# Performance work log

Measured on AMD Instinct MI355X. Metric: run time of the kernel, lower is better.

Reference implementation:

```python
import jax, jax.numpy as jnp
import numpy as np
import math

R1 = 1.0
R2 = 4.0
NBINS_XY = 4
NBINS_ZY = 4
PARTITIONS = NBINS_XY * NBINS_ZY * 2  # 32
TOPK = 200
TWO_PI = 2.0 * math.pi
PI = math.pi


def setup_inputs() -> dict:
    key = jax.random.key(0)
    k1, k2 = jax.random.split(key)
    # LiDAR-like coordinates, ~[-30, 30] meters
    sampled_vehicle_points = jax.random.normal(k1, (1024, 3), dtype=jnp.float32) * 20.0
    fusion_point = jax.random.normal(k2, (20000, 3), dtype=jnp.float32) * 20.0
    return {"sampled_vehicle_points": sampled_vehicle_points, "fusion_point": fusion_point}


def _compute_partitions_batch(q):
    # q: [S, K, 3]. rel[b, i, j] = q[b, j] - q[b, i]  (A.unsqueeze(1) - B.unsqueeze(2))
    rel = q[:, None, :, :] - q[:, :, None, :]  # [S, K, K, 3]
    angles_xy = jnp.fmod(jnp.arctan2(rel[..., 1], rel[..., 0]) + TWO_PI, TWO_PI)
    angles_zy = jnp.fmod(jnp.arctan2(rel[..., 1], rel[..., 2]) + TWO_PI, PI)
    xy_bins = jnp.floor(angles_xy / (TWO_PI / NBINS_XY))
    zy_bins = jnp.floor(angles_zy / (PI / NBINS_ZY))
    # hash(A, B, seed=NBINS_ZY): -1 where either < 0
    angle_ok = (xy_bins >= 0) & (zy_bins >= 0)
    angles_bins = jnp.where(angle_ok, xy_bins * NBINS_ZY + zy_bins, -1.0)
    D = jnp.sqrt(jnp.sum(rel * rel, axis=-1) + 1e-7)  # [S, K, K]
    dist_bins = jnp.where(D >= R2, 1.0, jnp.where(D >= R1, 0.0, -1.0))
    bin_ok = (dist_bins >= 0) & (angles_bins >= 0)
    bins = jnp.where(bin_ok, dist_bins * (NBINS_XY * NBINS_ZY) + angles_bins, -1.0)
    return bins  # [S, K, K] float, -1 for ignored


def reference(sampled_vehicle_points, fusion_point):
    # kNN query: K nearest fusion points for each sampled vehicle point
    d2 = jnp.sum(
        (sampled_vehicle_points[:, None, :] - fusion_point[None, :, :]) ** 2, axis=-1
    )  # [S, Nf]
    _, idx = jax.lax.top_k(-d2, TOPK)  # indices of TOPK smallest distances
    queried = fusion_point[idx]  # [S, K, 3]

    bins = _compute_partitions_batch(queried)  # [S, K, K]
    row0 = bins[:, 0, :]  # [S, K] — only row 0 is used by the loss
    # points_in_partition[s, p] = sum_j (row0[s, j] == p) + 1
    counts = jnp.sum(
        row0[:, :, None] == jnp.arange(PARTITIONS, dtype=bins.dtype)[None, None, :],
        axis=1,
    ).astype(jnp.float32) + 1.0  # [S, P]
    pip = counts / jnp.linalg.norm(counts, axis=-1, keepdims=True) * 4.0
    gt_dist = jax.nn.softmax(pip, axis=-1)
    return gt_dist
```

## Files before the change

### kernel.cpp

```cpp
#include <hip/hip_runtime.h>
#include <math.h>

#define KTOP 200
#define NPART 32
#define BLOCK 512
#define NHIST 2048
#define CAND_CAP 512
#define WCAP 512
#define CLIST_CAP 1536
#define SRANK_MIN 64u

__device__ __forceinline__ float d2_ref(float ax, float ay, float az,
                                        float bx, float by, float bz) {
    float dx = __fsub_rn(ax, bx), dy = __fsub_rn(ay, by), dz = __fsub_rn(az, bz);
    return __fadd_rn(__fadd_rn(__fmul_rn(dx, dx), __fmul_rn(dy, dy)), __fmul_rn(dz, dz));
}

__device__ __forceinline__ unsigned key_of(const float* __restrict__ fus, int j,
                                           float vx, float vy, float vz) {
    return __float_as_uint(d2_ref(vx, vy, vz, fus[3*j], fus[3*j+1], fus[3*j+2]));
}

__device__ __forceinline__ int compute_bin(float rx, float ry, float rz) {
    const float TWO_PI_F = (float)6.283185307179586;
    const float PI_F     = (float)3.141592653589793;
    const float XY_W     = (float)(6.283185307179586 / 4.0);
    const float ZY_W     = (float)(3.141592653589793 / 4.0);

    float d2 = __fadd_rn(__fadd_rn(__fmul_rn(rx, rx), __fmul_rn(ry, ry)), __fmul_rn(rz, rz));
    float D  = sqrtf(__fadd_rn(d2, 1e-7f));
    float dist_bin;
    if (D >= 4.0f)      dist_bin = 1.0f;
    else if (D >= 1.0f) dist_bin = 0.0f;
    else                return -1;

    float axy = fmodf(atan2f(ry, rx) + TWO_PI_F, TWO_PI_F);
    float azy = fmodf(atan2f(ry, rz) + TWO_PI_F, PI_F);
    float xyb = floorf(__fdiv_rn(axy, XY_W));
    float zyb = floorf(__fdiv_rn(azy, ZY_W));
    if (!(xyb >= 0.0f && zyb >= 0.0f)) return -1;
    float ab  = xyb * 4.0f + zyb;
    int bin = (int)(dist_bin * 16.0f + ab);
    return bin;
}

__global__ __launch_bounds__(BLOCK, 8)
void shape_context_kernel(const float* __restrict__ veh,
                          const float* __restrict__ fus,
                          float* __restrict__ out,
                          int nfus) {
    const int b   = blockIdx.x;
    const int tid = threadIdx.x;
    const int lane = tid & 63;
    const int wid  = tid >> 6;

    __shared__ unsigned int hist[NHIST];
    __shared__ unsigned long long clist[CLIST_CAP];
    __shared__ unsigned long long cand[CAND_CAP];
    __shared__ int wlist[WCAP];
    __shared__ unsigned int hist32[NPART];
    __shared__ unsigned int waveTot[BLOCK / 64];
    __shared__ unsigned int waveBase[BLOCK / 64];
    __shared__ unsigned int s_bucket, s_rem, s_bcount;
    __shared__ int s_candCount, s_wcount, s_clistCount;
    __shared__ float s_q0[3];
    __shared__ unsigned long long s_minPacked, s_lowBound;

    const float vx = veh[b * 3 + 0], vy = veh[b * 3 + 1], vz = veh[b * 3 + 2];
    const float4* fus4 = (const float4*)fus;
    const int ntrip = nfus >> 2;

    if (tid == 0) { s_minPacked = ~0ull; s_candCount = 0; s_wcount = 0; s_clistCount = 0; }
    for (int i = tid; i < NHIST; i += BLOCK) hist[i] = 0;
    if (tid < NPART) hist32[tid] = 0;
    __syncthreads();

    auto find_bucket = [&](unsigned remq) {
        if (tid == 0) s_bucket = 0xFFFFFFFFu;
        const int PER = NHIST / BLOCK;
        int base = tid * PER;
        unsigned p = 0;
        #pragma unroll
        for (int i = 0; i < PER; i++) p += hist[base + i];
        unsigned incl = p;
        #pragma unroll
        for (int d = 1; d < 64; d <<= 1) {
            unsigned n = __shfl_up(incl, d, 64);
            if (lane >= d) incl += n;
        }
        if (lane == 63) waveTot[wid] = incl;
        __syncthreads();
        if (tid == 0) {
            unsigned acc = 0;
            for (int w = 0; w < BLOCK / 64; w++) { waveBase[w] = acc; acc += waveTot[w]; }
        }
        __syncthreads();
        unsigned excl = waveBase[wid] + incl - p;
        if (excl < remq && remq <= excl + p) {
            unsigned cum = excl;
            #pragma unroll
            for (int i = 0; i < PER; i++) {
                unsigned c = hist[base + i];
                if (cum + c >= remq) { s_bucket = base + i; s_rem = remq - cum; s_bcount = c; break; }
                cum += c;
            }
        }
        __syncthreads();
    };

    auto push_l = [&](unsigned k, unsigned j) {
        int pos = atomicAdd(&s_clistCount, 1);
        if (pos < CLIST_CAP) clist[pos] = ((unsigned long long)k << 32) | j;
    };
    auto push_c = [&](unsigned k, unsigned j) {
        atomicAdd(&hist[k >> 21], 1u);
        int pos = atomicAdd(&s_clistCount, 1);
        if (pos < CLIST_CAP) clist[pos] = ((unsigned long long)k << 32) | j;
    };

    unsigned k0 = 0, k1 = 0, k2 = 0, k3 = 0;
    const bool t0v = (tid < ntrip);
    if (t0v) {
        float4 A = fus4[3 * tid], Bq = fus4[3 * tid + 1], Cq = fus4[3 * tid + 2];
        k0 = __float_as_uint(d2_ref(vx, vy, vz, A.x,  A.y,  A.z));
        k1 = __float_as_uint(d2_ref(vx, vy, vz, A.w,  Bq.x, Bq.y));
        k2 = __float_as_uint(d2_ref(vx, vy, vz, Bq.z, Bq.w, Cq.x));
        k3 = __float_as_uint(d2_ref(vx, vy, vz, Cq.y, Cq.z, Cq.w));
        atomicAdd(&hist[k0 >> 21], 1u);
        atomicAdd(&hist[k1 >> 21], 1u);
        atomicAdd(&hist[k2 >> 21], 1u);
        atomicAdd(&hist[k3 >> 21], 1u);
    }
    __syncthreads();

    unsigned srank;
    {
        long long sample = (long long)((ntrip < BLOCK) ? ntrip : BLOCK) * 4;
        if (sample >= (long long)nfus) {
            srank = KTOP;
        } else {
            unsigned s2 = (unsigned)(((long long)3 * KTOP * sample + nfus - 1) / nfus);
            srank = (s2 < SRANK_MIN) ? SRANK_MIN : s2;
        }
    }
    find_bucket(srank);
    const unsigned E = (s_bucket < NHIST) ? s_bucket : (NHIST - 1);
    const unsigned maxKey = ((E + 1u) << 21) - 1u;

    if (t0v) {
        unsigned jb = 4u * (unsigned)tid;
        int qm = (k0 <= maxKey ? 1 : 0) | (k1 <= maxKey ? 2 : 0)
               | (k2 <= maxKey ? 4 : 0) | (k3 <= maxKey ? 8 : 0);
        if (qm) {
            if (qm & 1) push_l(k0, jb + 0);
            if (qm & 2) push_l(k1, jb + 1);
            if (qm & 4) push_l(k2, jb + 2);
            if (qm & 8) push_l(k3, jb + 3);
        }
    }

    {
        int m = BLOCK + tid;
        bool valid = (m < ntrip);
        float4 A, Bq, Cq;
        if (valid) { A = fus4[3 * m]; Bq = fus4[3 * m + 1]; Cq = fus4[3 * m + 2]; }
        while (valid) {
            const int mn = m + BLOCK;
            const bool vnext = (mn < ntrip);
            float4 An, Bn, Cn;
            if (vnext) { An = fus4[3 * mn]; Bn = fus4[3 * mn + 1]; Cn = fus4[3 * mn + 2]; }

            unsigned q0k = __float_as_uint(d2_ref(vx, vy, vz, A.x,  A.y,  A.z));
            unsigned q1k = __float_as_uint(d2_ref(vx, vy, vz, A.w,  Bq.x, Bq.y));
            unsigned q2k = __float_as_uint(d2_ref(vx, vy, vz, Bq.z, Bq.w, Cq.x));
            unsigned q3k = __float_as_uint(d2_ref(vx, vy, vz, Cq.y, Cq.z, Cq.w));
            int qm = (q0k <= maxKey ? 1 : 0) | (q1k <= maxKey ? 2 : 0)
                   | (q2k <= maxKey ? 4 : 0) | (q3k <= maxKey ? 8 : 0);
            if (qm) {
                unsigned jb = 4u * (unsigned)m;
                if (qm & 1) push_c(q0k, jb + 0);
                if (qm & 2) push_c(q1k, jb + 1);
                if (qm & 4) push_c(q2k, jb + 2);
                if (qm & 8) push_c(q3k, jb + 3);
            }
            A = An; Bq = Bn; Cq = Cn; m = mn; valid = vnext;
        }
    }
    for (int j = (nfus & ~3) + tid; j < nfus; j += BLOCK) {
        unsigned k = key_of(fus, j, vx, vy, vz);
        if (k <= maxKey) push_c(k, (unsigned)j);
    }
    __syncthreads();

    find_bucket(KTOP);
    unsigned T = s_bucket;
    unsigned rem = s_rem;
    unsigned bcount = s_bcount;
    int shift = 21;
    const bool fastOK = (s_clistCount <= CLIST_CAP) && (T <= E);

    if (fastOK) {
        const int cn = s_clistCount;
        unsigned long long lm = ~0ull;
        for (int i = tid; i < cn; i += BLOCK) { unsigned long long p = clist[i]; lm = (p < lm) ? p : lm; }
        #pragma unroll
        for (int d = 32; d > 0; d >>= 1) {
            unsigned long long o = __shfl_xor(lm, d, 64);
            lm = (o < lm) ? o : lm;
        }
        if (lane == 0) atomicMin(&s_minPacked, lm);
        __syncthreads();
    } else {
        for (int i = tid; i < NHIST; i += BLOCK) hist[i] = 0;
        __syncthreads();
        unsigned long long lm = ~0ull;
        for (int j = tid; j < nfus; j += BLOCK) {
            unsigned k = key_of(fus, j, vx, vy, vz);
            atomicAdd(&hist[k >> 21], 1u);
            unsigned long long p = ((unsigned long long)k << 32) | (unsigned)j;
            lm = (p < lm) ? p : lm;
        }
        #pragma unroll
        for (int d = 32; d > 0; d >>= 1) {
            unsigned long long o = __shfl_xor(lm, d, 64);
            lm = (o < lm) ? o : lm;
        }
        if (lane == 0) atomicMin(&s_minPacked, lm);
        __syncthreads();
        find_bucket(KTOP);
        T = s_bucket; rem = s_rem; bcount = s_bcount;
    }

    if (tid == 0) {
        int idx0 = (int)(s_minPacked & 0xFFFFFFFFull);
        s_q0[0] = fus[idx0 * 3]; s_q0[1] = fus[idx0 * 3 + 1]; s_q0[2] = fus[idx0 * 3 + 2];
    }
    __syncthreads();
    const float q0x = s_q0[0], q0y = s_q0[1], q0z = s_q0[2];

    while (bcount > CAND_CAP && shift > 0) {
        int newshift = (shift > 11) ? (shift - 11) : 0;
        unsigned digmask = (1u << (shift - newshift)) - 1;
        for (int i = tid; i < NHIST; i += BLOCK) hist[i] = 0;
        __syncthreads();
        for (int j = tid; j < nfus; j += BLOCK) {
            unsigned k = key_of(fus, j, vx, vy, vz);
            if ((k >> shift) == T) atomicAdd(&hist[(k >> newshift) & digmask], 1u);
        }
        __syncthreads();
        find_bucket(rem);
        T = (T << (shift - newshift)) | s_bucket;
        rem = s_rem;
        bcount = s_bcount;
        shift = newshift;
    }

    if (fastOK && shift == 21) {
        const int cn = s_clistCount;
        for (int i = tid; i < cn; i += BLOCK) {
            unsigned long long p = clist[i];
            unsigned hi = (unsigned)(p >> 53);
            if (hi < T) {
                int pos = atomicAdd(&s_wcount, 1);
                if (pos < WCAP) wlist[pos] = (int)(p & 0xFFFFFFFFull);
            } else if (hi == T) {
                int pos = atomicAdd(&s_candCount, 1);
                if (pos < CAND_CAP) cand[pos] = p;
            }
        }
    } else {
        for (int j = tid; j < nfus; j += BLOCK) {
            unsigned k = key_of(fus, j, vx, vy, vz);
            unsigned hi = k >> shift;
            if (hi < T) { int pos = atomicAdd(&s_wcount, 1); if (pos < WCAP) wlist[pos] = j; }
            else if (hi == T) { int pos = atomicAdd(&s_candCount, 1); if (pos < CAND_CAP) cand[pos] = ((unsigned long long)k << 32) | (unsigned)j; }
        }
    }
    __syncthreads();

    const int cnt = s_candCount;
    if (cnt <= CAND_CAP) {
        for (int i = tid; i < cnt; i += BLOCK) {
            unsigned long long me = cand[i];
            int rank = 0;
            for (int k2 = 0; k2 < cnt; k2++) rank += (cand[k2] < me) ? 1 : 0;
            if (rank < (int)rem) {
                int pos = atomicAdd(&s_wcount, 1);
                if (pos < WCAP) wlist[pos] = (int)(me & 0xFFFFFFFFull);
            }
        }
    }
    __syncthreads();

    {
        int wc = s_wcount; if (wc > WCAP) wc = WCAP;
        for (int i = tid; i < wc; i += BLOCK) {
            int j = wlist[i];
            float fx = fus[3 * j], fy = fus[3 * j + 1], fz = fus[3 * j + 2];
            int bin = compute_bin(__fsub_rn(fx, q0x), __fsub_rn(fy, q0y), __fsub_rn(fz, q0z));
            if (bin >= 0 && bin < NPART) atomicAdd(&hist32[bin], 1u);
        }
    }
    __syncthreads();

    if (cnt > CAND_CAP) {
        if (tid == 0) s_lowBound = 0;
        __syncthreads();
        for (unsigned itx = 0; itx < rem; ++itx) {
            if (tid == 0) s_minPacked = ~0ull;
            __syncthreads();
            unsigned long long lowB = s_lowBound;
            unsigned long long lm = ~0ull;
            for (int j = tid; j < nfus; j += BLOCK) {
                unsigned k = key_of(fus, j, vx, vy, vz);
                if ((k >> shift) == T) {
                    unsigned long long p = ((unsigned long long)k << 32) | (unsigned)j;
                    if (p >= lowB && p < lm) lm = p;
                }
            }
            #pragma unroll
            for (int d = 32; d > 0; d >>= 1) {
                unsigned long long o = __shfl_xor(lm, d, 64);
                lm = (o < lm) ? o : lm;
            }
            if (lane == 0) atomicMin(&s_minPacked, lm);
            __syncthreads();
            if (tid == 0) {
                int jm = (int)(s_minPacked & 0xFFFFFFFFull);
                float fx = fus[jm * 3], fy = fus[jm * 3 + 1], fz = fus[jm * 3 + 2];
                int bin = compute_bin(__fsub_rn(fx, q0x), __fsub_rn(fy, q0y), __fsub_rn(fz, q0z));
                if (bin >= 0 && bin < NPART) hist32[bin] += 1u;
                s_lowBound = s_minPacked + 1;
            }
            __syncthreads();
        }
    }

    if (tid < NPART) {
        float c = (float)hist32[tid] + 1.0f;
        float ss = __fmul_rn(c, c);
        #pragma unroll
        for (int d = 16; d > 0; d >>= 1) ss += __shfl_xor(ss, d, 64);
        float v = __fmul_rn(__fdiv_rn(c, sqrtf(ss)), 4.0f);
        float mx = v;
        #pragma unroll
        for (int d = 16; d > 0; d >>= 1) mx = fmaxf(mx, __shfl_xor(mx, d, 64));
        float e = expf(v - mx);
        float sum = e;
        #pragma unroll
        for (int d = 16; d > 0; d >>= 1) sum += __shfl_xor(sum, d, 64);
        out[b * NPART + tid] = __fdiv_rn(e, sum);
    }
}

extern "C" void kernel_launch(void* const* d_in, const int* in_sizes, int n_in,
                              void* d_out, int out_size, void* d_ws, size_t ws_size,
                              hipStream_t stream) {
    const float* veh = (const float*)d_in[0];
    const float* fus = (const float*)d_in[1];
    float* out = (float*)d_out;
    int nveh = in_sizes[0] / 3;
    int nfus = in_sizes[1] / 3;
    shape_context_kernel<<<nveh, BLOCK, 0, stream>>>(veh, fus, out, nfus);
}
```

Baseline: 77.05 us.

## Stage fusion point chunks through LDS for coalesced loads in kNN scan

Replaces per-thread strided float4 triplet loads with fully coalesced chunk loads of 3*BLOCK float4s that are staged into a shared-memory pool, then each thread computes distances from LDS. The cand/wlist arrays are aliased onto that pool to keep LDS usage bounded. Launch bounds occupancy hint is lowered from 8 to 6. This adds two block barriers per chunk and removes the register-level prefetch of the next chunk, so latency hiding now depends on occupancy; the aliasing assumes cand/wlist are only used after the scan.

```diff
diff --git a/kernel.cpp b/kernel.cpp
--- a/kernel.cpp
+++ b/kernel.cpp
@@ -9,6 +9,8 @@
 #define WCAP 512
 #define CLIST_CAP 1536
 #define SRANK_MIN 64u
+#define CHUNK_PTS (4 * BLOCK)
+#define CHUNK_F4  (3 * BLOCK)
 
 __device__ __forceinline__ float d2_ref(float ax, float ay, float az,
                                         float bx, float by, float bz) {
@@ -44,7 +46,7 @@
     return bin;
 }
 
-__global__ __launch_bounds__(BLOCK, 8)
+__global__ __launch_bounds__(BLOCK, 6)
 void shape_context_kernel(const float* __restrict__ veh,
                           const float* __restrict__ fus,
                           float* __restrict__ out,
@@ -56,8 +58,7 @@
 
     __shared__ unsigned int hist[NHIST];
     __shared__ unsigned long long clist[CLIST_CAP];
-    __shared__ unsigned long long cand[CAND_CAP];
-    __shared__ int wlist[WCAP];
+    __shared__ __align__(16) char s_pool[CHUNK_F4 * 16];
     __shared__ unsigned int hist32[NPART];
     __shared__ unsigned int waveTot[BLOCK / 64];
     __shared__ unsigned int waveBase[BLOCK / 64];
@@ -66,9 +67,14 @@
     __shared__ float s_q0[3];
     __shared__ unsigned long long s_minPacked, s_lowBound;
 
+    float4* stage4 = (float4*)s_pool;
+    const float* stagef = (const float*)s_pool;
+    unsigned long long* cand = (unsigned long long*)s_pool;
+    int* wlist = (int*)(s_pool + CAND_CAP * 8);
+
     const float vx = veh[b * 3 + 0], vy = veh[b * 3 + 1], vz = veh[b * 3 + 2];
     const float4* fus4 = (const float4*)fus;
-    const int ntrip = nfus >> 2;
+    const int nfull = nfus / CHUNK_PTS;
 
     if (tid == 0) { s_minPacked = ~0ull; s_candCount = 0; s_wcount = 0; s_clistCount = 0; }
     for (int i = tid; i < NHIST; i += BLOCK) hist[i] = 0;
@@ -118,14 +124,21 @@
         if (pos < CLIST_CAP) clist[pos] = ((unsigned long long)k << 32) | j;
     };
 
+    auto key_at = [&](int p) {
+        float x = stagef[3 * p], y = stagef[3 * p + 1], z = stagef[3 * p + 2];
+        return __float_as_uint(d2_ref(vx, vy, vz, x, y, z));
+    };
+
+    const bool have0 = (nfull > 0);
     unsigned k0 = 0, k1 = 0, k2 = 0, k3 = 0;
-    const bool t0v = (tid < ntrip);
-    if (t0v) {
-        float4 A = fus4[3 * tid], Bq = fus4[3 * tid + 1], Cq = fus4[3 * tid + 2];
-        k0 = __float_as_uint(d2_ref(vx, vy, vz, A.x,  A.y,  A.z));
-        k1 = __float_as_uint(d2_ref(vx, vy, vz, A.w,  Bq.x, Bq.y));
-        k2 = __float_as_uint(d2_ref(vx, vy, vz, Bq.z, Bq.w, Cq.x));
-        k3 = __float_as_uint(d2_ref(vx, vy, vz, Cq.y, Cq.z, Cq.w));
+    if (have0) {
+        float4 r0 = fus4[tid], r1 = fus4[BLOCK + tid], r2 = fus4[2 * BLOCK + tid];
+        stage4[tid] = r0; stage4[BLOCK + tid] = r1; stage4[2 * BLOCK + tid] = r2;
+        __syncthreads();
+        k0 = key_at(tid);
+        k1 = key_at(tid + BLOCK);
+        k2 = key_at(tid + 2 * BLOCK);
+        k3 = key_at(tid + 3 * BLOCK);
         atomicAdd(&hist[k0 >> 21], 1u);
         atomicAdd(&hist[k1 >> 21], 1u);
         atomicAdd(&hist[k2 >> 21], 1u);
@@ -135,7 +148,7 @@
 
     unsigned srank;
     {
-        long long sample = (long long)((ntrip < BLOCK) ? ntrip : BLOCK) * 4;
+        long long sample = have0 ? (long long)CHUNK_PTS : 0;
         if (sample >= (long long)nfus) {
             srank = KTOP;
         } else {
@@ -147,46 +160,34 @@
     const unsigned E = (s_bucket < NHIST) ? s_bucket : (NHIST - 1);
     const unsigned maxKey = ((E + 1u) << 21) - 1u;
 
-    if (t0v) {
-        unsigned jb = 4u * (unsigned)tid;
-        int qm = (k0 <= maxKey ? 1 : 0) | (k1 <= maxKey ? 2 : 0)
-               | (k2 <= maxKey ? 4 : 0) | (k3 <= maxKey ? 8 : 0);
-        if (qm) {
-            if (qm & 1) push_l(k0, jb + 0);
-            if (qm & 2) push_l(k1, jb + 1);
-            if (qm & 4) push_l(k2, jb + 2);
-            if (qm & 8) push_l(k3, jb + 3);
-        }
-    }
-
-    {
-        int m = BLOCK + tid;
-        bool valid = (m < ntrip);
-        float4 A, Bq, Cq;
-        if (valid) { A = fus4[3 * m]; Bq = fus4[3 * m + 1]; Cq = fus4[3 * m + 2]; }
-        while (valid) {
-            const int mn = m + BLOCK;
-            const bool vnext = (mn < ntrip);
-            float4 An, Bn, Cn;
-            if (vnext) { An = fus4[3 * mn]; Bn = fus4[3 * mn + 1]; Cn = fus4[3 * mn + 2]; }
-
-            unsigned q0k = __float_as_uint(d2_ref(vx, vy, vz, A.x,  A.y,  A.z));
-            unsigned q1k = __float_as_uint(d2_ref(vx, vy, vz, A.w,  Bq.x, Bq.y));
-            unsigned q2k = __float_as_uint(d2_ref(vx, vy, vz, Bq.z, Bq.w, Cq.x));
-            unsigned q3k = __float_as_uint(d2_ref(vx, vy, vz, Cq.y, Cq.z, Cq.w));
-            int qm = (q0k <= maxKey ? 1 : 0) | (q1k <= maxKey ? 2 : 0)
-                   | (q2k <= maxKey ? 4 : 0) | (q3k <= maxKey ? 8 : 0);
-            if (qm) {
-                unsigned jb = 4u * (unsigned)m;
-                if (qm & 1) push_c(q0k, jb + 0);
-                if (qm & 2) push_c(q1k, jb + 1);
-                if (qm & 4) push_c(q2k, jb + 2);
-                if (qm & 8) push_c(q3k, jb + 3);
-            }
-            A = An; Bq = Bn; Cq = Cn; m = mn; valid = vnext;
-        }
-    }
-    for (int j = (nfus & ~3) + tid; j < nfus; j += BLOCK) {
+    if (have0) {
+        if (k0 <= maxKey) push_l(k0, (unsigned)tid);
+        if (k1 <= maxKey) push_l(k1, (unsigned)(tid + BLOCK));
+        if (k2 <= maxKey) push_l(k2, (unsigned)(tid + 2 * BLOCK));
+        if (k3 <= maxKey) push_l(k3, (unsigned)(tid + 3 * BLOCK));
+    }
+
+    for (int c = 1; c < nfull; ++c) {
+        const int f4b = c * CHUNK_F4;
+        float4 r0 = fus4[f4b + tid];
+        float4 r1 = fus4[f4b + BLOCK + tid];
+        float4 r2 = fus4[f4b + 2 * BLOCK + tid];
+        __syncthreads();
+        stage4[tid] = r0; stage4[BLOCK + tid] = r1; stage4[2 * BLOCK + tid] = r2;
+        __syncthreads();
+        const int jb = c * CHUNK_PTS;
+        unsigned q0 = key_at(tid);
+        unsigned q1 = key_at(tid + BLOCK);
+        unsigned q2 = key_at(tid + 2 * BLOCK);
+        unsigned q3 = key_at(tid + 3 * BLOCK);
+        if ((q0 <= maxKey) | (q1 <= maxKey) | (q2 <= maxKey) | (q3 <= maxKey)) {
+            if (q0 <= maxKey) push_c(q0, (unsigned)(jb + tid));
+            if (q1 <= maxKey) push_c(q1, (unsigned)(jb + tid + BLOCK));
+            if (q2 <= maxKey) push_c(q2, (unsigned)(jb + tid + 2 * BLOCK));
+            if (q3 <= maxKey) push_c(q3, (unsigned)(jb + tid + 3 * BLOCK));
+        }
+    }
+    for (int j = nfull * CHUNK_PTS + tid; j < nfus; j += BLOCK) {
         unsigned k = key_of(fus, j, vx, vy, vz);
         if (k <= maxKey) push_c(k, (unsigned)j);
     }
```

New measurement: 89.23 us. 15.8% more time.

## Process four query points per block to reuse fusion-point loads

Applied to the files above, without the earlier changes.

Each block now handles four vehicle points instead of one. Every loaded fusion-point triple is scored against all four queries, with a separate histogram and candidate list kept per query. The block size rises from 512 to 1024 threads and the grid shrinks to a quarter. This cuts global load traffic and per-block setup, at the cost of more shared memory, more registers, only 256 blocks for the GPU, and the per-query selection tails running one after another.

```diff
diff --git a/kernel.cpp b/kernel.cpp
--- a/kernel.cpp
+++ b/kernel.cpp
@@ -3,7 +3,8 @@
 
 #define KTOP 200
 #define NPART 32
-#define BLOCK 512
+#define BLOCK 1024
+#define NV 4
 #define NHIST 2048
 #define CAND_CAP 512
 #define WCAP 512
@@ -14,6 +15,11 @@
                                         float bx, float by, float bz) {
     float dx = __fsub_rn(ax, bx), dy = __fsub_rn(ay, by), dz = __fsub_rn(az, bz);
     return __fadd_rn(__fadd_rn(__fmul_rn(dx, dx), __fmul_rn(dy, dy)), __fmul_rn(dz, dz));
+}
+
+__device__ __forceinline__ unsigned key2(float cx, float cy, float cz,
+                                         float px, float py, float pz) {
+    return __float_as_uint(d2_ref(cx, cy, cz, px, py, pz));
 }
 
 __device__ __forceinline__ unsigned key_of(const float* __restrict__ fus, int j,
@@ -44,44 +50,51 @@
     return bin;
 }
 
-__global__ __launch_bounds__(BLOCK, 8)
+__global__ __launch_bounds__(BLOCK, 4)
 void shape_context_kernel(const float* __restrict__ veh,
                           const float* __restrict__ fus,
                           float* __restrict__ out,
-                          int nfus) {
-    const int b   = blockIdx.x;
-    const int tid = threadIdx.x;
+                          int nfus, int nveh) {
+    const int b    = blockIdx.x;
+    const int tid  = threadIdx.x;
     const int lane = tid & 63;
     const int wid  = tid >> 6;
-
-    __shared__ unsigned int hist[NHIST];
-    __shared__ unsigned long long clist[CLIST_CAP];
+    const int vbase = b * NV;
+
+    __shared__ unsigned int hist[NV][NHIST];
+    __shared__ unsigned long long clist[NV][CLIST_CAP];
     __shared__ unsigned long long cand[CAND_CAP];
     __shared__ int wlist[WCAP];
     __shared__ unsigned int hist32[NPART];
     __shared__ unsigned int waveTot[BLOCK / 64];
     __shared__ unsigned int waveBase[BLOCK / 64];
     __shared__ unsigned int s_bucket, s_rem, s_bcount;
-    __shared__ int s_candCount, s_wcount, s_clistCount;
+    __shared__ int s_candCount, s_wcount, s_clistCount[NV];
+    __shared__ unsigned int s_E[NV];
     __shared__ float s_q0[3];
     __shared__ unsigned long long s_minPacked, s_lowBound;
 
-    const float vx = veh[b * 3 + 0], vy = veh[b * 3 + 1], vz = veh[b * 3 + 2];
+    const int vi0 = min(vbase + 0, nveh - 1), vi1 = min(vbase + 1, nveh - 1),
+              vi2 = min(vbase + 2, nveh - 1), vi3 = min(vbase + 3, nveh - 1);
+    const float cAx = veh[vi0*3], cAy = veh[vi0*3+1], cAz = veh[vi0*3+2];
+    const float cBx = veh[vi1*3], cBy = veh[vi1*3+1], cBz = veh[vi1*3+2];
+    const float cCx = veh[vi2*3], cCy = veh[vi2*3+1], cCz = veh[vi2*3+2];
+    const float cDx = veh[vi3*3], cDy = veh[vi3*3+1], cDz = veh[vi3*3+2];
+
     const float4* fus4 = (const float4*)fus;
     const int ntrip = nfus >> 2;
 
-    if (tid == 0) { s_minPacked = ~0ull; s_candCount = 0; s_wcount = 0; s_clistCount = 0; }
-    for (int i = tid; i < NHIST; i += BLOCK) hist[i] = 0;
-    if (tid < NPART) hist32[tid] = 0;
-    __syncthreads();
-
-    auto find_bucket = [&](unsigned remq) {
+    for (int i = tid; i < NV * NHIST; i += BLOCK) ((unsigned*)hist)[i] = 0;
+    if (tid < NV) s_clistCount[tid] = 0;
+    __syncthreads();
+
+    auto find_bucket = [&](const unsigned* h, unsigned remq) {
         if (tid == 0) s_bucket = 0xFFFFFFFFu;
         const int PER = NHIST / BLOCK;
         int base = tid * PER;
         unsigned p = 0;
         #pragma unroll
-        for (int i = 0; i < PER; i++) p += hist[base + i];
+        for (int i = 0; i < PER; i++) p += h[base + i];
         unsigned incl = p;
         #pragma unroll
         for (int d = 1; d < 64; d <<= 1) {
@@ -100,7 +113,7 @@
             unsigned cum = excl;
             #pragma unroll
             for (int i = 0; i < PER; i++) {
-                unsigned c = hist[base + i];
+                unsigned c = h[base + i];
                 if (cum + c >= remq) { s_bucket = base + i; s_rem = remq - cum; s_bcount = c; break; }
                 cum += c;
             }
@@ -108,216 +121,156 @@
         __syncthreads();
     };
 
-    auto push_l = [&](unsigned k, unsigned j) {
-        int pos = atomicAdd(&s_clistCount, 1);
-        if (pos < CLIST_CAP) clist[pos] = ((unsigned long long)k << 32) | j;
+    auto push_l = [&](int v, unsigned k, unsigned j) {
+        int pos = atomicAdd(&s_clistCount[v], 1);
+        if (pos < CLIST_CAP) clist[v][pos] = ((unsigned long long)k << 32) | j;
     };
-    auto push_c = [&](unsigned k, unsigned j) {
-        atomicAdd(&hist[k >> 21], 1u);
-        int pos = atomicAdd(&s_clistCount, 1);
-        if (pos < CLIST_CAP) clist[pos] = ((unsigned long long)k << 32) | j;
+    auto push_c = [&](int v, unsigned k, unsigned j) {
+        atomicAdd(&hist[v][k >> 21], 1u);
+        int pos = atomicAdd(&s_clistCount[v], 1);
+        if (pos < CLIST_CAP) clist[v][pos] = ((unsigned long long)k << 32) | j;
     };
 
-    unsigned k0 = 0, k1 = 0, k2 = 0, k3 = 0;
-    const bool t0v = (tid < ntrip);
+    const int t0n = (ntrip < BLOCK) ? ntrip : BLOCK;
+    const bool t0v = (tid < t0n);
+    float p0x=0,p0y=0,p0z=0, p1x=0,p1y=0,p1z=0, p2x=0,p2y=0,p2z=0, p3x=0,p3y=0,p3z=0;
+    unsigned sA0=0,sA1=0,sA2=0,sA3=0, sB0=0,sB1=0,sB2=0,sB3=0;
+    unsigned sC0=0,sC1=0,sC2=0,sC3=0, sD0=0,sD1=0,sD2=0,sD3=0;
     if (t0v) {
-        float4 A = fus4[3 * tid], Bq = fus4[3 * tid + 1], Cq = fus4[3 * tid + 2];
-        k0 = __float_as_uint(d2_ref(vx, vy, vz, A.x,  A.y,  A.z));
-        k1 = __float_as_uint(d2_ref(vx, vy, vz, A.w,  Bq.x, Bq.y));
-        k2 = __float_as_uint(d2_ref(vx, vy, vz, Bq.z, Bq.w, Cq.x));
-        k3 = __float_as_uint(d2_ref(vx, vy, vz, Cq.y, Cq.z, Cq.w));
-        atomicAdd(&hist[k0 >> 21], 1u);
-        atomicAdd(&hist[k1 >> 21], 1u);
-        atomicAdd(&hist[k2 >> 21], 1u);
-        atomicAdd(&hist[k3 >> 21], 1u);
+        float4 A = fus4[3*tid], Bq = fus4[3*tid+1], Cq = fus4[3*tid+2];
+        p0x=A.x;  p0y=A.y;  p0z=A.z;
+        p1x=A.w;  p1y=Bq.x; p1z=Bq.y;
+        p2x=Bq.z; p2y=Bq.w; p2z=Cq.x;
+        p3x=Cq.y; p3y=Cq.z; p3z=Cq.w;
+        sA0=key2(cAx,cAy,cAz,p0x,p0y,p0z); sA1=key2(cAx,cAy,cAz,p1x,p1y,p1z);
+        sA2=key2(cAx,cAy,cAz,p2x,p2y,p2z); sA3=key2(cAx,cAy,cAz,p3x,p3y,p3z);
+        sB0=key2(cBx,cBy,cBz,p0x,p0y,p0z); sB1=key2(cBx,cBy,cBz,p1x,p1y,p1z);
+        sB2=key2(cBx,cBy,cBz,p2x,p2y,p2z); sB3=key2(cBx,cBy,cBz,p3x,p3y,p3z);
+        sC0=key2(cCx,cCy,cCz,p0x,p0y,p0z); sC1=key2(cCx,cCy,cCz,p1x,p1y,p1z);
+        sC2=key2(cCx,cCy,cCz,p2x,p2y,p2z); sC3=key2(cCx,cCy,cCz,p3x,p3y,p3z);
+        sD0=key2(cDx,cDy,cDz,p0x,p0y,p0z); sD1=key2(cDx,cDy,cDz,p1x,p1y,p1z);
+        sD2=key2(cDx,cDy,cDz,p2x,p2y,p2z); sD3=key2(cDx,cDy,cDz,p3x,p3y,p3z);
+        atomicAdd(&hist[0][sA0>>21],1u); atomicAdd(&hist[0][sA1>>21],1u);
+        atomicAdd(&hist[0][sA2>>21],1u); atomicAdd(&hist[0][sA3>>21],1u);
+        atomicAdd(&hist[1][sB0>>21],1u); atomicAdd(&hist[1][sB1>>21],1u);
+        atomicAdd(&hist[1][sB2>>21],1u); atomicAdd(&hist[1][sB3>>21],1u);
+        atomicAdd(&hist[2][sC0>>21],1u); atomicAdd(&hist[2][sC1>>21],1u);
+        atomicAdd(&hist[2][sC2>>21],1u); atomicAdd(&hist[2][sC3>>21],1u);
+        atomicAdd(&hist[3][sD0>>21],1u); atomicAdd(&hist[3][sD1>>21],1u);
+        atomicAdd(&hist[3][sD2>>21],1u); atomicAdd(&hist[3][sD3>>21],1u);
     }
     __syncthreads();
 
     unsigned srank;
     {
-        long long sample = (long long)((ntrip < BLOCK) ? ntrip : BLOCK) * 4;
+        long long sample = 4LL * t0n;
         if (sample >= (long long)nfus) {
             srank = KTOP;
         } else {
-            unsigned s2 = (unsigned)(((long long)3 * KTOP * sample + nfus - 1) / nfus);
+            unsigned s2 = (unsigned)((3LL * KTOP * sample + nfus - 1) / nfus);
             srank = (s2 < SRANK_MIN) ? SRANK_MIN : s2;
         }
     }
-    find_bucket(srank);
-    const unsigned E = (s_bucket < NHIST) ? s_bucket : (NHIST - 1);
-    const unsigned maxKey = ((E + 1u) << 21) - 1u;
+    find_bucket(hist[0], srank);
+    const unsigned E0 = (s_bucket < NHIST) ? s_bucket : (NHIST-1);
+    if (tid == 0) s_E[0] = E0;
+    __syncthreads();
+    find_bucket(hist[1], srank);
+    const unsigned E1 = (s_bucket < NHIST) ? s_bucket : (NHIST-1);
+    if (tid == 0) s_E[1] = E1;
+    __syncthreads();
+    find_bucket(hist[2], srank);
+    const unsigned E2 = (s_bucket < NHIST) ? s_bucket : (NHIST-1);
+    if (tid == 0) s_E[2] = E2;
+    __syncthreads();
+    find_bucket(hist[3], srank);
+    const unsigned E3 = (s_bucket < NHIST) ? s_bucket : (NHIST-1);
+    if (tid == 0) s_E[3] = E3;
+    __syncthreads();
+    const unsigned mk0 = ((E0+1u)<<21)-1u, mk1 = ((E1+1u)<<21)-1u;
+    const unsigned mk2 = ((E2+1u)<<21)-1u, mk3 = ((E3+1u)<<21)-1u;
 
     if (t0v) {
         unsigned jb = 4u * (unsigned)tid;
-        int qm = (k0 <= maxKey ? 1 : 0) | (k1 <= maxKey ? 2 : 0)
-               | (k2 <= maxKey ? 4 : 0) | (k3 <= maxKey ? 8 : 0);
-        if (qm) {
-            if (qm & 1) push_l(k0, jb + 0);
-            if (qm & 2) push_l(k1, jb + 1);
-            if (qm & 4) push_l(k2, jb + 2);
-            if (qm & 8) push_l(k3, jb + 3);
-        }
-    }
-
-    {
-        int m = BLOCK + tid;
-        bool valid = (m < ntrip);
-        float4 A, Bq, Cq;
-        if (valid) { A = fus4[3 * m]; Bq = fus4[3 * m + 1]; Cq = fus4[3 * m + 2]; }
-        while (valid) {
-            const int mn = m + BLOCK;
-            const bool vnext = (mn < ntrip);
-            float4 An, Bn, Cn;
-            if (vnext) { An = fus4[3 * mn]; Bn = fus4[3 * mn + 1]; Cn = fus4[3 * mn + 2]; }
-
-            unsigned q0k = __float_as_uint(d2_ref(vx, vy, vz, A.x,  A.y,  A.z));
-            unsigned q1k = __float_as_uint(d2_ref(vx, vy, vz, A.w,  Bq.x, Bq.y));
-            unsigned q2k = __float_as_uint(d2_ref(vx, vy, vz, Bq.z, Bq.w, Cq.x));
-            unsigned q3k = __float_as_uint(d2_ref(vx, vy, vz, Cq.y, Cq.z, Cq.w));
-            int qm = (q0k <= maxKey ? 1 : 0) | (q1k <= maxKey ? 2 : 0)
-                   | (q2k <= maxKey ? 4 : 0) | (q3k <= maxKey ? 8 : 0);
-            if (qm) {
-                unsigned jb = 4u * (unsigned)m;
-                if (qm & 1) push_c(q0k, jb + 0);
-                if (qm & 2) push_c(q1k, jb + 1);
-                if (qm & 4) push_c(q2k, jb + 2);
-                if (qm & 8) push_c(q3k, jb + 3);
-            }
-            A = An; Bq = Bn; Cq = Cn; m = mn; valid = vnext;
+        if (sA0<=mk0) push_l(0,sA0,jb+0); if (sA1<=mk0) push_l(0,sA1,jb+1);
+        if (sA2<=mk0) push_l(0,sA2,jb+2); if (sA3<=mk0) push_l(0,sA3,jb+3);
+        if (sB0<=mk1) push_l(1,sB0,jb+0); if (sB1<=mk1) push_l(1,sB1,jb+1);
+        if (sB2<=mk1) push_l(1,sB2,jb+2); if (sB3<=mk1) push_l(1,sB3,jb+3);
+        if (sC0<=mk2) push_l(2,sC0,jb+0); if (sC1<=mk2) push_l(2,sC1,jb+1);
+        if (sC2<=mk2) push_l(2,sC2,jb+2); if (sC3<=mk2) push_l(2,sC3,jb+3);
+        if (sD0<=mk3) push_l(3,sD0,jb+0); if (sD1<=mk3) push_l(3,sD1,jb+1);
+        if (sD2<=mk3) push_l(3,sD2,jb+2); if (sD3<=mk3) push_l(3,sD3,jb+3);
+    }
+
+    for (int m = BLOCK + tid; m < ntrip; m += BLOCK) {
+        float4 A = fus4[3*m], Bq = fus4[3*m+1], Cq = fus4[3*m+2];
+        float x0=A.x,  y0=A.y,  z0=A.z;
+        float x1=A.w,  y1=Bq.x, z1=Bq.y;
+        float x2=Bq.z, y2=Bq.w, z2=Cq.x;
+        float x3=Cq.y, y3=Cq.z, z3=Cq.w;
+        unsigned jb = 4u * (unsigned)m;
+        {
+            unsigned k0=key2(cAx,cAy,cAz,x0,y0,z0), k1=key2(cAx,cAy,cAz,x1,y1,z1);
+            unsigned k2=key2(cAx,cAy,cAz,x2,y2,z2), k3=key2(cAx,cAy,cAz,x3,y3,z3);
+            if ((k0<=mk0)|(k1<=mk0)|(k2<=mk0)|(k3<=mk0)) {
+                if (k0<=mk0) push_c(0,k0,jb+0); if (k1<=mk0) push_c(0,k1,jb+1);
+                if (k2<=mk0) push_c(0,k2,jb+2); if (k3<=mk0) push_c(0,k3,jb+3);
+            }
+        }
+        {
+            unsigned k0=key2(cBx,cBy,cBz,x0,y0,z0), k1=key2(cBx,cBy,cBz,x1,y1,z1);
+            unsigned k2=key2(cBx,cBy,cBz,x2,y2,z2), k3=key2(cBx,cBy,cBz,x3,y3,z3);
+            if ((k0<=mk1)|(k1<=mk1)|(k2<=mk1)|(k3<=mk1)) {
+                if (k0<=mk1) push_c(1,k0,jb+0); if (k1<=mk1) push_c(1,k1,jb+1);
+                if (k2<=mk1) push_c(1,k2,jb+2); if (k3<=mk1) push_c(1,k3,jb+3);
+            }
+        }
+        {
+            unsigned k0=key2(cCx,cCy,cCz,x0,y0,z0), k1=key2(cCx,cCy,cCz,x1,y1,z1);
+            unsigned k2=key2(cCx,cCy,cCz,x2,y2,z2), k3=key2(cCx,cCy,cCz,x3,y3,z3);
+            if ((k0<=mk2)|(k1<=mk2)|(k2<=mk2)|(k3<=mk2)) {
+                if (k0<=mk2) push_c(2,k0,jb+0); if (k1<=mk2) push_c(2,k1,jb+1);
+                if (k2<=mk2) push_c(2,k2,jb+2); if (k3<=mk2) push_c(2,k3,jb+3);
+            }
+        }
+        {
+            unsigned k0=key2(cDx,cDy,cDz,x0,y0,z0), k1=key2(cDx,cDy,cDz,x1,y1,z1);
+            unsigned k2=key2(cDx,cDy,cDz,x2,y2,z2), k3=key2(cDx,cDy,cDz,x3,y3,z3);
+            if ((k0<=mk3)|(k1<=mk3)|(k2<=mk3)|(k3<=mk3)) {
+                if (k0<=mk3) push_c(3,k0,jb+0); if (k1<=mk3) push_c(3,k1,jb+1);
+                if (k2<=mk3) push_c(3,k2,jb+2); if (k3<=mk3) push_c(3,k3,jb+3);
+            }
         }
     }
     for (int j = (nfus & ~3) + tid; j < nfus; j += BLOCK) {
-        unsigned k = key_of(fus, j, vx, vy, vz);
-        if (k <= maxKey) push_c(k, (unsigned)j);
-    }
-    __syncthreads();
-
-    find_bucket(KTOP);
-    unsigned T = s_bucket;
-    unsigned rem = s_rem;
-    unsigned bcount = s_bcount;
-    int shift = 21;
-    const bool fastOK = (s_clistCount <= CLIST_CAP) && (T <= E);
-
-    if (fastOK) {
-        const int cn = s_clistCount;
-        unsigned long long lm = ~0ull;
-        for (int i = tid; i < cn; i += BLOCK) { unsigned long long p = clist[i]; lm = (p < lm) ? p : lm; }
-        #pragma unroll
-        for (int d = 32; d > 0; d >>= 1) {
-            unsigned long long o = __shfl_xor(lm, d, 64);
-            lm = (o < lm) ? o : lm;
-        }
-        if (lane == 0) atomicMin(&s_minPacked, lm);
-        __syncthreads();
-    } else {
-        for (int i = tid; i < NHIST; i += BLOCK) hist[i] = 0;
-        __syncthreads();
-        unsigned long long lm = ~0ull;
-        for (int j = tid; j < nfus; j += BLOCK) {
-            unsigned k = key_of(fus, j, vx, vy, vz);
-            atomicAdd(&hist[k >> 21], 1u);
-            unsigned long long p = ((unsigned long long)k << 32) | (unsigned)j;
-            lm = (p < lm) ? p : lm;
-        }
-        #pragma unroll
-        for (int d = 32; d > 0; d >>= 1) {
-            unsigned long long o = __shfl_xor(lm, d, 64);
-            lm = (o < lm) ? o : lm;
-        }
-        if (lane == 0) atomicMin(&s_minPacked, lm);
-        __syncthreads();
-        find_bucket(KTOP);
-        T = s_bucket; rem = s_rem; bcount = s_bcount;
-    }
-
-    if (tid == 0) {
-        int idx0 = (int)(s_minPacked & 0xFFFFFFFFull);
-        s_q0[0] = fus[idx0 * 3]; s_q0[1] = fus[idx0 * 3 + 1]; s_q0[2] = fus[idx0 * 3 + 2];
-    }
-    __syncthreads();
-    const float q0x = s_q0[0], q0y = s_q0[1], q0z = s_q0[2];
-
-    while (bcount > CAND_CAP && shift > 0) {
-        int newshift = (shift > 11) ? (shift - 11) : 0;
-        unsigned digmask = (1u << (shift - newshift)) - 1;
-        for (int i = tid; i < NHIST; i += BLOCK) hist[i] = 0;
-        __syncthreads();
-        for (int j = tid; j < nfus; j += BLOCK) {
-            unsigned k = key_of(fus, j, vx, vy, vz);
-            if ((k >> shift) == T) atomicAdd(&hist[(k >> newshift) & digmask], 1u);
-        }
-        __syncthreads();
-        find_bucket(rem);
-        T = (T << (shift - newshift)) | s_bucket;
-        rem = s_rem;
-        bcount = s_bcount;
-        shift = newshift;
-    }
-
-    if (fastOK && shift == 21) {
-        const int cn = s_clistCount;
-        for (int i = tid; i < cn; i += BLOCK) {
-            unsigned long long p = clist[i];
-            unsigned hi = (unsigned)(p >> 53);
-            if (hi < T) {
-                int pos = atomicAdd(&s_wcount, 1);
-                if (pos < WCAP) wlist[pos] = (int)(p & 0xFFFFFFFFull);
-            } else if (hi == T) {
-                int pos = atomicAdd(&s_candCount, 1);
-                if (pos < CAND_CAP) cand[pos] = p;
-            }
-        }
-    } else {
-        for (int j = tid; j < nfus; j += BLOCK) {
-            unsigned k = key_of(fus, j, vx, vy, vz);
-            unsigned hi = k >> shift;
-            if (hi < T) { int pos = atomicAdd(&s_wcount, 1); if (pos < WCAP) wlist[pos] = j; }
-            else if (hi == T) { int pos = atomicAdd(&s_candCount, 1); if (pos < CAND_CAP) cand[pos] = ((unsigned long long)k << 32) | (unsigned)j; }
-        }
-    }
-    __syncthreads();
-
-    const int cnt = s_candCount;
-    if (cnt <= CAND_CAP) {
-        for (int i = tid; i < cnt; i += BLOCK) {
-            unsigned long long me = cand[i];
-            int rank = 0;
-            for (int k2 = 0; k2 < cnt; k2++) rank += (cand[k2] < me) ? 1 : 0;
-            if (rank < (int)rem) {
-                int pos = atomicAdd(&s_wcount, 1);
-                if (pos < WCAP) wlist[pos] = (int)(me & 0xFFFFFFFFull);
-            }
-        }
-    }
-    __syncthreads();
-
-    {
-        int wc = s_wcount; if (wc > WCAP) wc = WCAP;
-        for (int i = tid; i < wc; i += BLOCK) {
-            int j = wlist[i];
-            float fx = fus[3 * j], fy = fus[3 * j + 1], fz = fus[3 * j + 2];
-            int bin = compute_bin(__fsub_rn(fx, q0x), __fsub_rn(fy, q0y), __fsub_rn(fz, q0z));
-            if (bin >= 0 && bin < NPART) atomicAdd(&hist32[bin], 1u);
-        }
-    }
-    __syncthreads();
-
-    if (cnt > CAND_CAP) {
-        if (tid == 0) s_lowBound = 0;
-        __syncthreads();
-        for (unsigned itx = 0; itx < rem; ++itx) {
-            if (tid == 0) s_minPacked = ~0ull;
-            __syncthreads();
-            unsigned long long lowB = s_lowBound;
+        float fx = fus[3*j], fy = fus[3*j+1], fz = fus[3*j+2];
+        unsigned k;
+        k = key2(cAx,cAy,cAz,fx,fy,fz); if (k<=mk0) push_c(0,k,(unsigned)j);
+        k = key2(cBx,cBy,cBz,fx,fy,fz); if (k<=mk1) push_c(1,k,(unsigned)j);
+        k = key2(cCx,cCy,cCz,fx,fy,fz); if (k<=mk2) push_c(2,k,(unsigned)j);
+        k = key2(cDx,cDy,cDz,fx,fy,fz); if (k<=mk3) push_c(3,k,(unsigned)j);
+    }
+    __syncthreads();
+
+    for (int v = 0; v < NV; ++v) {
+        unsigned* hv = hist[v];
+        unsigned long long* clv = clist[v];
+        const int vi = min(vbase + v, nveh - 1);
+        const float vxv = veh[vi*3], vyv = veh[vi*3+1], vzv = veh[vi*3+2];
+
+        if (tid == 0) { s_minPacked = ~0ull; s_candCount = 0; s_wcount = 0; }
+        if (tid < NPART) hist32[tid] = 0;
+        __syncthreads();
+
+        find_bucket(hv, KTOP);
+        unsigned T = s_bucket, rem = s_rem, bcount = s_bcount;
+        int shift = 21;
+        const bool fastOK = (s_clistCount[v] <= CLIST_CAP) && (T <= s_E[v]);
+
+        if (fastOK) {
+            const int cn = s_clistCount[v];
             unsigned long long lm = ~0ull;
-            for (int j = tid; j < nfus; j += BLOCK) {
-                unsigned k = key_of(fus, j, vx, vy, vz);
-                if ((k >> shift) == T) {
-                    unsigned long long p = ((unsigned long long)k << 32) | (unsigned)j;
-                    if (p >= lowB && p < lm) lm = p;
-                }
-            }
+            for (int i = tid; i < cn; i += BLOCK) { unsigned long long p = clv[i]; lm = (p < lm) ? p : lm; }
             #pragma unroll
             for (int d = 32; d > 0; d >>= 1) {
                 unsigned long long o = __shfl_xor(lm, d, 64);
@@ -325,31 +278,148 @@
             }
             if (lane == 0) atomicMin(&s_minPacked, lm);
             __syncthreads();
-            if (tid == 0) {
-                int jm = (int)(s_minPacked & 0xFFFFFFFFull);
-                float fx = fus[jm * 3], fy = fus[jm * 3 + 1], fz = fus[jm * 3 + 2];
+        } else {
+            for (int i = tid; i < NHIST; i += BLOCK) hv[i] = 0;
+            __syncthreads();
+            unsigned long long lm = ~0ull;
+            for (int j = tid; j < nfus; j += BLOCK) {
+                unsigned k = key_of(fus, j, vxv, vyv, vzv);
+                atomicAdd(&hv[k >> 21], 1u);
+                unsigned long long p = ((unsigned long long)k << 32) | (unsigned)j;
+                lm = (p < lm) ? p : lm;
+            }
+            #pragma unroll
+            for (int d = 32; d > 0; d >>= 1) {
+                unsigned long long o = __shfl_xor(lm, d, 64);
+                lm = (o < lm) ? o : lm;
+            }
+            if (lane == 0) atomicMin(&s_minPacked, lm);
+            __syncthreads();
+            find_bucket(hv, KTOP);
+            T = s_bucket; rem = s_rem; bcount = s_bcount;
+        }
+
+        if (tid == 0) {
+            int idx0 = (int)(s_minPacked & 0xFFFFFFFFull);
+            s_q0[0] = fus[idx0*3]; s_q0[1] = fus[idx0*3+1]; s_q0[2] = fus[idx0*3+2];
+        }
+        __syncthreads();
+        const float q0x = s_q0[0], q0y = s_q0[1], q0z = s_q0[2];
+
+        while (bcount > CAND_CAP && shift > 0) {
+            int newshift = (shift > 11) ? (shift - 11) : 0;
+            unsigned digmask = (1u << (shift - newshift)) - 1;
+            for (int i = tid; i < NHIST; i += BLOCK) hv[i] = 0;
+            __syncthreads();
+            for (int j = tid; j < nfus; j += BLOCK) {
+                unsigned k = key_of(fus, j, vxv, vyv, vzv);
+                if ((k >> shift) == T) atomicAdd(&hv[(k >> newshift) & digmask], 1u);
+            }
+            __syncthreads();
+            find_bucket(hv, rem);
+            T = (T << (shift - newshift)) | s_bucket;
+            rem = s_rem;
+            bcount = s_bcount;
+            shift = newshift;
+        }
+
+        if (fastOK && shift == 21) {
+            const int cn = s_clistCount[v];
+            for (int i = tid; i < cn; i += BLOCK) {
+                unsigned long long p = clv[i];
+                unsigned hi = (unsigned)(p >> 53);
+                if (hi < T) {
+                    int pos = atomicAdd(&s_wcount, 1);
+                    if (pos < WCAP) wlist[pos] = (int)(p & 0xFFFFFFFFull);
+                } else if (hi == T) {
+                    int pos = atomicAdd(&s_candCount, 1);
+                    if (pos < CAND_CAP) cand[pos] = p;
+                }
+            }
+        } else {
+            for (int j = tid; j < nfus; j += BLOCK) {
+                unsigned k = key_of(fus, j, vxv, vyv, vzv);
+                unsigned hi = k >> shift;
+                if (hi < T) { int pos = atomicAdd(&s_wcount, 1); if (pos < WCAP) wlist[pos] = j; }
+                else if (hi == T) { int pos = atomicAdd(&s_candCount, 1); if (pos < CAND_CAP) cand[pos] = ((unsigned long long)k << 32) | (unsigned)j; }
+            }
+        }
+        __syncthreads();
+
+        const int cnt = s_candCount;
+        if (cnt <= CAND_CAP) {
+            for (int i = tid; i < cnt; i += BLOCK) {
+                unsigned long long me = cand[i];
+                int rank = 0;
+                for (int k2 = 0; k2 < cnt; k2++) rank += (cand[k2] < me) ? 1 : 0;
+                if (rank < (int)rem) {
+                    int pos = atomicAdd(&s_wcount, 1);
+                    if (pos < WCAP) wlist[pos] = (int)(me & 0xFFFFFFFFull);
+                }
+            }
+        }
+        __syncthreads();
+
+        {
+            int wc = s_wcount; if (wc > WCAP) wc = WCAP;
+            for (int i = tid; i < wc; i += BLOCK) {
+                int j = wlist[i];
+                float fx = fus[3*j], fy = fus[3*j+1], fz = fus[3*j+2];
                 int bin = compute_bin(__fsub_rn(fx, q0x), __fsub_rn(fy, q0y), __fsub_rn(fz, q0z));
-                if (bin >= 0 && bin < NPART) hist32[bin] += 1u;
-                s_lowBound = s_minPacked + 1;
-            }
-            __syncthreads();
-        }
-    }
-
-    if (tid < NPART) {
-        float c = (float)hist32[tid] + 1.0f;
-        float ss = __fmul_rn(c, c);
-        #pragma unroll
-        for (int d = 16; d > 0; d >>= 1) ss += __shfl_xor(ss, d, 64);
-        float v = __fmul_rn(__fdiv_rn(c, sqrtf(ss)), 4.0f);
-        float mx = v;
-        #pragma unroll
-        for (int d = 16; d > 0; d >>= 1) mx = fmaxf(mx, __shfl_xor(mx, d, 64));
-        float e = expf(v - mx);
-        float sum = e;
-        #pragma unroll
-        for (int d = 16; d > 0; d >>= 1) sum += __shfl_xor(sum, d, 64);
-        out[b * NPART + tid] = __fdiv_rn(e, sum);
+                if (bin >= 0 && bin < NPART) atomicAdd(&hist32[bin], 1u);
+            }
+        }
+        __syncthreads();
+
+        if (cnt > CAND_CAP) {
+            if (tid == 0) s_lowBound = 0;
+            __syncthreads();
+            for (unsigned itx = 0; itx < rem; ++itx) {
+                if (tid == 0) s_minPacked = ~0ull;
+                __syncthreads();
+                unsigned long long lowB = s_lowBound;
+                unsigned long long lm = ~0ull;
+                for (int j = tid; j < nfus; j += BLOCK) {
+                    unsigned k = key_of(fus, j, vxv, vyv, vzv);
+                    if ((k >> shift) == T) {
+                        unsigned long long p = ((unsigned long long)k << 32) | (unsigned)j;
+                        if (p >= lowB && p < lm) lm = p;
+                    }
+                }
+                #pragma unroll
+                for (int d = 32; d > 0; d >>= 1) {
+                    unsigned long long o = __shfl_xor(lm, d, 64);
+                    lm = (o < lm) ? o : lm;
+                }
+                if (lane == 0) atomicMin(&s_minPacked, lm);
+                __syncthreads();
+                if (tid == 0) {
+                    int jm = (int)(s_minPacked & 0xFFFFFFFFull);
+                    float fx = fus[jm*3], fy = fus[jm*3+1], fz = fus[jm*3+2];
+                    int bin = compute_bin(__fsub_rn(fx, q0x), __fsub_rn(fy, q0y), __fsub_rn(fz, q0z));
+                    if (bin >= 0 && bin < NPART) hist32[bin] += 1u;
+                    s_lowBound = s_minPacked + 1;
+                }
+                __syncthreads();
+            }
+        }
+
+        if (tid < NPART) {
+            float c = (float)hist32[tid] + 1.0f;
+            float ss = __fmul_rn(c, c);
+            #pragma unroll
+            for (int d = 16; d > 0; d >>= 1) ss += __shfl_xor(ss, d, 64);
+            float vv = __fmul_rn(__fdiv_rn(c, sqrtf(ss)), 4.0f);
+            float mx = vv;
+            #pragma unroll
+            for (int d = 16; d > 0; d >>= 1) mx = fmaxf(mx, __shfl_xor(mx, d, 64));
+            float e = expf(vv - mx);
+            float sum = e;
+            #pragma unroll
+            for (int d = 16; d > 0; d >>= 1) sum += __shfl_xor(sum, d, 64);
+            if (vbase + v < nveh) out[(vbase + v) * NPART + tid] = __fdiv_rn(e, sum);
+        }
+        __syncthreads();
     }
 }
 
@@ -361,5 +431,6 @@
     float* out = (float*)d_out;
     int nveh = in_sizes[0] / 3;
     int nfus = in_sizes[1] / 3;
-    shape_context_kernel<<<nveh, BLOCK, 0, stream>>>(veh, fus, out, nfus);
-}
+    int nblocks = (nveh + NV - 1) / NV;
+    shape_context_kernel<<<nblocks, BLOCK, 0, stream>>>(veh, fus, out, nfus, nveh);
+}
```

After: 96.08 us. +24.7%, slower.
